# Optimization experiments

Hardware: AMD Instinct MI355X
Metric: run time of the kernel (lower is better)

Reference implementation:

```python
import jax, jax.numpy as jnp
import numpy as np

IDIM = 128
C = 3
NB_SAMPLES = 128
R = 32768
SH_C0 = 0.28209479177387814
SH_C1 = 0.4886025119029199
SH_C2 = np.array([1.0925484305920792, -1.0925484305920792, 0.31539156525252005,
                  -1.0925484305920792, 0.5462742152960396], dtype=np.float32)


def eval_sh_bases(d):
    # d: (R,3) unit directions -> (R,9) degree-2 real SH basis
    x, y, z = d[:, 0], d[:, 1], d[:, 2]
    return jnp.stack([
        jnp.full_like(x, SH_C0),
        -SH_C1 * y, SH_C1 * z, -SH_C1 * x,
        SH_C2[0] * x * y, SH_C2[1] * y * z,
        SH_C2[2] * (2.0 * z * z - x * x - y * y),
        SH_C2[3] * x * z, SH_C2[4] * (x * x - y * y)], axis=-1)


def trilerp(pts, grid):
    # pts: (N,3) in voxel coords (box_min=0, delta_voxel=1); grid: (D,D,D,F)
    D = grid.shape[0]
    p = jnp.clip(pts, 0.0, D - 1 - 1e-4)
    i0 = jnp.floor(p).astype(jnp.int32)
    w = p - i0.astype(p.dtype)          # (N,3) fractional weights
    i1 = jnp.minimum(i0 + 1, D - 1)
    out = jnp.zeros((pts.shape[0], grid.shape[-1]), dtype=p.dtype)
    for dx in (0, 1):
        wx = w[:, 0] if dx else 1.0 - w[:, 0]
        ix = i1[:, 0] if dx else i0[:, 0]
        for dy in (0, 1):
            wy = w[:, 1] if dy else 1.0 - w[:, 1]
            iy = i1[:, 1] if dy else i0[:, 1]
            for dz in (0, 1):
                wz = w[:, 2] if dz else 1.0 - w[:, 2]
                iz = i1[:, 2] if dz else i0[:, 2]
                out = out + (wx * wy * wz)[:, None] * grid[ix, iy, iz]
    return out


def setup_inputs() -> dict:
    key = jax.random.key(0)
    k = jax.random.split(key, 6)
    x = jax.random.uniform(k[0], (R, 3), jnp.float32) * (IDIM - 1)
    d = jax.random.normal(k[1], (R, 3), jnp.float32)
    d = d / jnp.linalg.norm(d, axis=1, keepdims=True)
    tmin = jax.random.uniform(k[2], (R,), jnp.float32) * 5.0
    tmax = tmin + 20.0 + jax.random.uniform(k[3], (R,), jnp.float32) * 80.0
    grid = jax.random.uniform(k[4], (IDIM, IDIM, IDIM, 9 * C), jnp.float32)
    opacity = jax.random.uniform(k[5], (IDIM, IDIM, IDIM, 1), jnp.float32)
    return {"x": x, "d": d, "tmin": tmin, "tmax": tmax, "grid": grid, "opacity": opacity}


def reference(x, d, tmin, tmax, grid, opacity):
    nb_rays = x.shape[0]
    # samples = arange(0.05, 0.95, 1/nb_samples): S entries
    S = int(np.floor(0.9 * NB_SAMPLES - 1e-6)) + 1
    base = 0.05 + jnp.arange(S, dtype=x.dtype) / NB_SAMPLES            # (S,)
    samples = (tmax - tmin)[:, None] * base[None, :] + tmin[:, None]   # (R,S)
    pts = x[:, None, :] + samples[..., None] * d[:, None, :]           # (R,S,3)
    sh = eval_sh_bases(d)                                              # (R,9)
    flat = pts.reshape(-1, 3)
    coeffs = trilerp(flat, grid).reshape(nb_rays, S, C, 9)             # (R,S,C,9)
    op = jnp.clip(trilerp(flat, opacity), 0.0, 100000.0).reshape(nb_rays, S)
    harm = coeffs * sh[:, None, None, :]                               # (R,S,C,9)
    samples_color = jnp.clip(harm.sum(axis=3) + 0.5, 0.0, 100000.0)    # (R,S,C)
    deltas = samples[:, 1:] - samples[:, :-1]                          # (R,S-1)
    dts = -(deltas * op[:, :-1])
    cum = jnp.concatenate([jnp.zeros((nb_rays, 1), dtype=x.dtype),
                           jnp.cumsum(dts, axis=1)[:, :-1]], axis=1)
    w = jnp.exp(cum) * (1.0 - jnp.exp(dts))                            # (R,S-1)
    rays_color = jnp.sum(w[..., None] * samples_color[:, :-1, :], axis=1)  # (R,C)
    return rays_color
```

## Files before the change

kernel.cpp:

```cpp
#include <hip/hip_runtime.h>

#define NS 115
#define WEPS 5e-5f
#define LOG_TSKIP -6.9078f
#define NCELLS (128*128*128)
#define PACK_BYTES ((size_t)NCELLS * 64)
#define NEED_BYTES PACK_BYTES
#define PACK_BLOCKS 2048
#define PACK_THREADS (PACK_BLOCKS * 256)
#define PACK_ITERS ((NCELLS * 4) / PACK_THREADS)

typedef float f32x4 __attribute__((ext_vector_type(4)));
typedef float f32x2 __attribute__((ext_vector_type(2)));
typedef _Float16 h16x8 __attribute__((ext_vector_type(8)));
typedef _Float16 h16x4 __attribute__((ext_vector_type(4)));

struct SH9 { float a,b,c,d,e,f,g,h,i; };

__device__ __forceinline__ f32x4 load4(const float* p) { f32x4 v; __builtin_memcpy(&v, p, 16); return v; }
__device__ __forceinline__ f32x2 load2(const float* p) { f32x2 v; __builtin_memcpy(&v, p, 8);  return v; }
__device__ __forceinline__ h16x8 load8h(const _Float16* p) { h16x8 v; __builtin_memcpy(&v, p, 16); return v; }
__device__ __forceinline__ f32x4 ntload4(const float* p) {
    return __builtin_nontemporal_load((const f32x4*)p);
}

__device__ __forceinline__ void pos_to_cell(float px, float py, float pz,
                                            int& ibase, float* wxs, float* wys, float* wzs) {
    px = fminf(fmaxf(px, 0.0f), 126.9999f);
    py = fminf(fmaxf(py, 0.0f), 126.9999f);
    pz = fminf(fmaxf(pz, 0.0f), 126.9999f);
    int ix = (int)px, iy = (int)py, iz = (int)pz;
    float wx = px - (float)ix, wy = py - (float)iy, wz = pz - (float)iz;
    ibase = (ix << 14) + (iy << 7) + iz;
    wxs[0] = 1.0f - wx; wxs[1] = wx;
    wys[0] = 1.0f - wy; wys[1] = wy;
    wzs[0] = 1.0f - wz; wzs[1] = wz;
}

__device__ __forceinline__ float eval_op(float px, float py, float pz,
                                         const float* __restrict__ opa) {
    int ibase; float wxs[2], wys[2], wzs[2];
    pos_to_cell(px, py, pz, ibase, wxs, wys, wzs);
    float op = 0.0f;
    #pragma unroll
    for (int cx = 0; cx < 2; ++cx)
    #pragma unroll
    for (int cy = 0; cy < 2; ++cy) {
        int idx = ibase + (cx << 14) + (cy << 7);
        f32x2 pr = load2(opa + idx);
        float wxy = wxs[cx] * wys[cy];
        op = fmaf(wxy * wzs[0], pr.x, op);
        op = fmaf(wxy * wzs[1], pr.y, op);
    }
    return fminf(fmaxf(op, 0.0f), 100000.0f);
}

__device__ __forceinline__ void eval_color_f(float px, float py, float pz,
                                             const float* __restrict__ grid,
                                             const SH9& sh,
                                             float& cr, float& cg, float& cb) {
    int ibase; float wxs[2], wys[2], wzs[2];
    pos_to_cell(px, py, pz, ibase, wxs, wys, wzs);
    float r = 0.0f, g = 0.0f, b = 0.0f;
    #pragma unroll
    for (int cx = 0; cx < 2; ++cx)
    #pragma unroll
    for (int cy = 0; cy < 2; ++cy)
    #pragma unroll
    for (int cz = 0; cz < 2; ++cz) {
        int idx = ibase + (cx << 14) + (cy << 7) + cz;
        float wc = wxs[cx] * wys[cy] * wzs[cz];
        const float* cp = grid + (size_t)idx * 27;
        f32x4 v0 = load4(cp);
        f32x4 v1 = load4(cp + 4);
        f32x4 v2 = load4(cp + 8);
        f32x4 v3 = load4(cp + 12);
        f32x4 v4 = load4(cp + 16);
        f32x4 v5 = load4(cp + 20);
        f32x4 v6 = load4(cp + 23);
        float c0 = sh.a*v0.x + sh.b*v0.y + sh.c*v0.z + sh.d*v0.w
                 + sh.e*v1.x + sh.f*v1.y + sh.g*v1.z + sh.h*v1.w + sh.i*v2.x;
        float c1 = sh.a*v2.y + sh.b*v2.z + sh.c*v2.w + sh.d*v3.x
                 + sh.e*v3.y + sh.f*v3.z + sh.g*v3.w + sh.h*v4.x + sh.i*v4.y;
        float c2 = sh.a*v4.z + sh.b*v4.w + sh.c*v5.x + sh.d*v5.y
                 + sh.e*v5.z + sh.f*v5.w + sh.g*v6.y + sh.h*v6.z + sh.i*v6.w;
        r = fmaf(wc, c0, r);
        g = fmaf(wc, c1, g);
        b = fmaf(wc, c2, b);
    }
    cr = fminf(fmaxf(r + 0.5f, 0.0f), 100000.0f);
    cg = fminf(fmaxf(g + 0.5f, 0.0f), 100000.0f);
    cb = fminf(fmaxf(b + 0.5f, 0.0f), 100000.0f);
}

__device__ __forceinline__ float wave_incl_scan(float v, int lane) {
    #pragma unroll
    for (int off = 1; off < 64; off <<= 1) {
        float n = __shfl_up(v, (unsigned)off, 64);
        if (lane >= off) v += n;
    }
    return v;
}

__device__ __forceinline__ SH9 make_sh(float ddx, float ddy, float ddz) {
    SH9 sh;
    sh.a = 0.28209479177387814f;
    sh.b = -0.4886025119029199f * ddy;
    sh.c =  0.4886025119029199f * ddz;
    sh.d = -0.4886025119029199f * ddx;
    sh.e =  1.0925484305920792f * ddx * ddy;
    sh.f = -1.0925484305920792f * ddy * ddz;
    sh.g =  0.31539156525252005f * (2.0f*ddz*ddz - ddx*ddx - ddy*ddy);
    sh.h = -1.0925484305920792f * ddx * ddz;
    sh.i =  0.5462742152960396f * (ddx*ddx - ddy*ddy);
    return sh;
}

__device__ __forceinline__ void pack_one(const float* __restrict__ grid,
                                         _Float16* __restrict__ pack, int o) {
    int cell = o >> 2;
    int q = o & 3;
    int base = cell * 27;
    int offa = base + ((q == 3) ? 23 : q * 8);
    int offb = (q == 3) ? offa : offa + 4;
    f32x4 a = ntload4(grid + offa);
    f32x4 b = ntload4(grid + offb);
    h16x8 out;
    if (q == 3) {
        out[0] = (_Float16)a.y; out[1] = (_Float16)a.z; out[2] = (_Float16)a.w;
        out[3] = (_Float16)0.f; out[4] = (_Float16)0.f; out[5] = (_Float16)0.f;
        out[6] = (_Float16)0.f; out[7] = (_Float16)0.f;
    } else {
        out[0] = (_Float16)a.x; out[1] = (_Float16)a.y; out[2] = (_Float16)a.z; out[3] = (_Float16)a.w;
        out[4] = (_Float16)b.x; out[5] = (_Float16)b.y; out[6] = (_Float16)b.z; out[7] = (_Float16)b.w;
    }
    __builtin_memcpy(pack + ((size_t)o << 3), &out, 16);
}

__global__ __launch_bounds__(256) void pack_kernel(
    const float* __restrict__ grid, _Float16* __restrict__ pack)
{
    const int tid = blockIdx.x * 256 + threadIdx.x;
    #pragma unroll 1
    for (int i = 0; i < PACK_ITERS; i += 8) {
        #pragma unroll
        for (int j = 0; j < 8; ++j)
            pack_one(grid, pack, tid + (i + j) * PACK_THREADS);
    }
}

__global__ __launch_bounds__(256) void fused_color_kernel(
    const float* __restrict__ x, const float* __restrict__ d,
    const float* __restrict__ tmin, const float* __restrict__ tmax,
    const float* __restrict__ opa, const _Float16* __restrict__ pack,
    float* __restrict__ out, int nrays)
{
    int gtid = blockIdx.x * blockDim.x + threadIdx.x;
    int ray = __builtin_amdgcn_readfirstlane(gtid >> 6);
    int lane = threadIdx.x & 63;
    if (ray >= nrays) return;
    int qd  = lane >> 2;
    int sub = lane & 3;

    float ox = x[3*ray+0], oy = x[3*ray+1], oz = x[3*ray+2];
    float ddx = d[3*ray+0], ddy = d[3*ray+1], ddz = d[3*ray+2];
    float t0 = tmin[ray];
    float range = tmax[ray] - t0;
    float delta = range * 0.0078125f;
    SH9 sh = make_sh(ddx, ddy, ddz);

    float tt = range * (0.05f + (float)lane * 0.0078125f) + t0;
    {
    }
    float px0 = ox + tt*ddx, py0 = oy + tt*ddy, pz0 = oz + tt*ddz;
    float opv = eval_op(px0, py0, pz0, opa);
    float dts = -delta * opv;
    float incl = wave_incl_scan(dts, lane);
    float cum = incl - dts;
    float total0 = __shfl(incl, 63, 64);
    float w0 = __expf(cum) * (1.0f - __expf(dts));

    float w1 = 0.0f;
    if (total0 > LOG_TSKIP) {
        int s1 = 64 + lane;
        float dts1 = 0.0f;
        if (s1 < NS) {
            float t1s = range * (0.05f + (float)s1 * 0.0078125f) + t0;
            float qx = ox + t1s*ddx, qy = oy + t1s*ddy, qz = oz + t1s*ddz;
            dts1 = -delta * eval_op(qx, qy, qz, opa);
        }
        float incl1 = wave_incl_scan(dts1, lane);
        float cum1 = total0 + incl1 - dts1;
        w1 = __expf(cum1) * (1.0f - __expf(dts1));
    }

    float s00,s01,s02,s03,s04,s05,s06,s07;
    float s10,s11,s12,s13,s14,s15,s16,s17;
    if (sub == 0) {
        s00=sh.a;s01=sh.b;s02=sh.c;s03=sh.d;s04=sh.e;s05=sh.f;s06=sh.g;s07=sh.h;
        s10=0.f;s11=0.f;s12=0.f;s13=0.f;s14=0.f;s15=0.f;s16=0.f;s17=0.f;
    } else if (sub == 1) {
        s00=sh.i;s01=0.f;s02=0.f;s03=0.f;s04=0.f;s05=0.f;s06=0.f;s07=0.f;
        s10=0.f;s11=sh.a;s12=sh.b;s13=sh.c;s14=sh.d;s15=sh.e;s16=sh.f;s17=sh.g;
    } else if (sub == 2) {
        s00=sh.h;s01=sh.i;s02=0.f;s03=0.f;s04=0.f;s05=0.f;s06=0.f;s07=0.f;
        s10=0.f;s11=0.f;s12=sh.a;s13=sh.b;s14=sh.c;s15=sh.d;s16=sh.e;s17=sh.f;
    } else {
        s00=sh.g;s01=sh.h;s02=sh.i;s03=0.f;s04=0.f;s05=0.f;s06=0.f;s07=0.f;
        s10=0.f;s11=0.f;s12=0.f;s13=0.f;s14=0.f;s15=0.f;s16=0.f;s17=0.f;
    }

    unsigned long long b0 = __ballot(w0 > WEPS);
    unsigned long long b1 = __ballot(w1 > WEPS);

    float accR = 0.0f, accG = 0.0f, accB = 0.0f;

    #pragma unroll 1
    for (int p = 0; p < 8; ++p) {
        unsigned long long bsel = (p < 4) ? b0 : b1;
        int shl = (p & 3) << 4;
        if (((bsel >> shl) & 0xFFFFull) == 0) continue;
        int s = (p << 4) + qd;
        float ws = __shfl((p < 4) ? w0 : w1, s & 63, 64);
        if (ws > WEPS) {
            float st = range * (0.05f + (float)s * 0.0078125f) + t0;
            float px = ox + st*ddx, py = oy + st*ddy, pz = oz + st*ddz;
            int ibase; float wxs[2], wys[2], wzs[2];
            pos_to_cell(px, py, pz, ibase, wxs, wys, wzs);
            float d0a = 0.0f, d1a = 0.0f;
            #pragma unroll
            for (int cx = 0; cx < 2; ++cx)
            #pragma unroll
            for (int cy = 0; cy < 2; ++cy)
            #pragma unroll
            for (int cz = 0; cz < 2; ++cz) {
                int idx = ibase + (cx << 14) + (cy << 7) + cz;
                float wc = wxs[cx] * wys[cy] * wzs[cz];
                const _Float16* cp = pack + ((size_t)idx << 5) + (sub << 3);
                h16x8 v = load8h(cp);
                float f0=(float)v[0], f1=(float)v[1], f2=(float)v[2], f3=(float)v[3];
                float f4=(float)v[4], f5=(float)v[5], f6=(float)v[6], f7=(float)v[7];
                float e0 = s00*f0 + s01*f1 + s02*f2 + s03*f3
                         + s04*f4 + s05*f5 + s06*f6 + s07*f7;
                float e1 = s10*f0 + s11*f1 + s12*f2 + s13*f3
                         + s14*f4 + s15*f5 + s16*f6 + s17*f7;
                d0a = fmaf(wc, e0, d0a);
                d1a = fmaf(wc, e1, d1a);
            }
            float rp = (sub < 2)  ? d0a : 0.0f;
            float gp = (sub == 1) ? d1a : ((sub == 2) ? d0a : 0.0f);
            float bp = (sub == 2) ? d1a : ((sub == 3) ? d0a : 0.0f);
            rp += __shfl_xor(rp, 1, 64); rp += __shfl_xor(rp, 2, 64);
            gp += __shfl_xor(gp, 1, 64); gp += __shfl_xor(gp, 2, 64);
            bp += __shfl_xor(bp, 1, 64); bp += __shfl_xor(bp, 2, 64);
            float cr = fminf(fmaxf(rp + 0.5f, 0.0f), 100000.0f);
            float cg = fminf(fmaxf(gp + 0.5f, 0.0f), 100000.0f);
            float cb = fminf(fmaxf(bp + 0.5f, 0.0f), 100000.0f);
            accR = fmaf(ws, cr, accR);
            accG = fmaf(ws, cg, accG);
            accB = fmaf(ws, cb, accB);
        }
    }

    #pragma unroll
    for (int off = 4; off < 64; off <<= 1) {
        accR += __shfl_xor(accR, off, 64);
        accG += __shfl_xor(accG, off, 64);
        accB += __shfl_xor(accB, off, 64);
    }
    if (lane == 0) {
        out[3*ray+0] = accR;
        out[3*ray+1] = accG;
        out[3*ray+2] = accB;
    }
}

__global__ __launch_bounds__(256) void rf_fallback(
    const float* __restrict__ x, const float* __restrict__ d,
    const float* __restrict__ tmin, const float* __restrict__ tmax,
    const float* __restrict__ grid, const float* __restrict__ opa,
    float* __restrict__ out, int nrays)
{
    int gtid = blockIdx.x * blockDim.x + threadIdx.x;
    int ray = __builtin_amdgcn_readfirstlane(gtid >> 6);
    int lane = threadIdx.x & 63;
    if (ray >= nrays) return;

    float ox = x[3*ray+0], oy = x[3*ray+1], oz = x[3*ray+2];
    float ddx = d[3*ray+0], ddy = d[3*ray+1], ddz = d[3*ray+2];
    float t0 = tmin[ray], t1 = tmax[ray];
    float range = t1 - t0;
    float delta = range * 0.0078125f;
    SH9 sh = make_sh(ddx, ddy, ddz);

    float accR = 0.0f, accG = 0.0f, accB = 0.0f;
    {
        float tt = range * (0.05f + (float)lane * 0.0078125f) + t0;
        float px = ox + tt*ddx, py = oy + tt*ddy, pz = oz + tt*ddz;
        float opv = eval_op(px, py, pz, opa);
        float dts = -delta * opv;
        float incl = wave_incl_scan(dts, lane);
        float cum = incl - dts;
        float total0 = __shfl(incl, 63, 64);
        float w = __expf(cum) * (1.0f - __expf(dts));
        if (w > WEPS) {
            float cr, cg, cb;
            eval_color_f(px, py, pz, grid, sh, cr, cg, cb);
            accR = w * cr; accG = w * cg; accB = w * cb;
        }
        if (total0 > LOG_TSKIP) {
            int s1 = 64 + lane;
            float dts1 = 0.0f;
            float px1 = 0.f, py1 = 0.f, pz1 = 0.f;
            if (s1 < NS) {
                float t1s = range * (0.05f + (float)s1 * 0.0078125f) + t0;
                px1 = ox + t1s*ddx; py1 = oy + t1s*ddy; pz1 = oz + t1s*ddz;
                dts1 = -delta * eval_op(px1, py1, pz1, opa);
            }
            float incl1 = wave_incl_scan(dts1, lane);
            float cum1 = total0 + incl1 - dts1;
            float w1 = __expf(cum1) * (1.0f - __expf(dts1));
            if (w1 > WEPS) {
                float cr, cg, cb;
                eval_color_f(px1, py1, pz1, grid, sh, cr, cg, cb);
                accR = fmaf(w1, cr, accR);
                accG = fmaf(w1, cg, accG);
                accB = fmaf(w1, cb, accB);
            }
        }
    }
    #pragma unroll
    for (int off = 32; off > 0; off >>= 1) {
        accR += __shfl_xor(accR, off, 64);
        accG += __shfl_xor(accG, off, 64);
        accB += __shfl_xor(accB, off, 64);
    }
    if (lane == 0) {
        out[3*ray+0] = accR;
        out[3*ray+1] = accG;
        out[3*ray+2] = accB;
    }
}

extern "C" void kernel_launch(void* const* d_in, const int* in_sizes, int n_in,
                              void* d_out, int out_size, void* d_ws, size_t ws_size,
                              hipStream_t stream) {
    const float* x    = (const float*)d_in[0];
    const float* d    = (const float*)d_in[1];
    const float* tmin = (const float*)d_in[2];
    const float* tmax = (const float*)d_in[3];
    const float* grid = (const float*)d_in[4];
    const float* opa  = (const float*)d_in[5];
    float* out = (float*)d_out;

    int nrays = in_sizes[0] / 3;
    int blocks = (nrays * 64 + 255) / 256;

    if (ws_size >= NEED_BYTES) {
        _Float16* pack = (_Float16*)d_ws;
        pack_kernel<<<PACK_BLOCKS, 256, 0, stream>>>(grid, pack);
        fused_color_kernel<<<blocks, 256, 0, stream>>>(x, d, tmin, tmax, opa, pack, out, nrays);
    } else {
        rf_fallback<<<blocks, 256, 0, stream>>>(x, d, tmin, tmax, grid, opa, out, nrays);
    }
}
```

Before: 391.7 us.

## Drop fp16 grid pre-pack kernel and gather fp32 coefficients directly

```diff
diff --git a/kernel.cpp b/kernel.cpp
--- a/kernel.cpp
+++ b/kernel.cpp
@@ -3,26 +3,14 @@
 #define NS 115
 #define WEPS 5e-5f
 #define LOG_TSKIP -6.9078f
-#define NCELLS (128*128*128)
-#define PACK_BYTES ((size_t)NCELLS * 64)
-#define NEED_BYTES PACK_BYTES
-#define PACK_BLOCKS 2048
-#define PACK_THREADS (PACK_BLOCKS * 256)
-#define PACK_ITERS ((NCELLS * 4) / PACK_THREADS)
 
 typedef float f32x4 __attribute__((ext_vector_type(4)));
 typedef float f32x2 __attribute__((ext_vector_type(2)));
-typedef _Float16 h16x8 __attribute__((ext_vector_type(8)));
-typedef _Float16 h16x4 __attribute__((ext_vector_type(4)));
 
 struct SH9 { float a,b,c,d,e,f,g,h,i; };
 
 __device__ __forceinline__ f32x4 load4(const float* p) { f32x4 v; __builtin_memcpy(&v, p, 16); return v; }
 __device__ __forceinline__ f32x2 load2(const float* p) { f32x2 v; __builtin_memcpy(&v, p, 8);  return v; }
-__device__ __forceinline__ h16x8 load8h(const _Float16* p) { h16x8 v; __builtin_memcpy(&v, p, 16); return v; }
-__device__ __forceinline__ f32x4 ntload4(const float* p) {
-    return __builtin_nontemporal_load((const f32x4*)p);
-}
 
 __device__ __forceinline__ void pos_to_cell(float px, float py, float pz,
                                             int& ibase, float* wxs, float* wys, float* wzs) {
@@ -53,44 +41,6 @@
         op = fmaf(wxy * wzs[1], pr.y, op);
     }
     return fminf(fmaxf(op, 0.0f), 100000.0f);
-}
-
-__device__ __forceinline__ void eval_color_f(float px, float py, float pz,
-                                             const float* __restrict__ grid,
-                                             const SH9& sh,
-                                             float& cr, float& cg, float& cb) {
-    int ibase; float wxs[2], wys[2], wzs[2];
-    pos_to_cell(px, py, pz, ibase, wxs, wys, wzs);
-    float r = 0.0f, g = 0.0f, b = 0.0f;
-    #pragma unroll
-    for (int cx = 0; cx < 2; ++cx)
-    #pragma unroll
-    for (int cy = 0; cy < 2; ++cy)
-    #pragma unroll
-    for (int cz = 0; cz < 2; ++cz) {
-        int idx = ibase + (cx << 14) + (cy << 7) + cz;
-        float wc = wxs[cx] * wys[cy] * wzs[cz];
-        const float* cp = grid + (size_t)idx * 27;
-        f32x4 v0 = load4(cp);
-        f32x4 v1 = load4(cp + 4);
-        f32x4 v2 = load4(cp + 8);
-        f32x4 v3 = load4(cp + 12);
-        f32x4 v4 = load4(cp + 16);
-        f32x4 v5 = load4(cp + 20);
-        f32x4 v6 = load4(cp + 23);
-        float c0 = sh.a*v0.x + sh.b*v0.y + sh.c*v0.z + sh.d*v0.w
-                 + sh.e*v1.x + sh.f*v1.y + sh.g*v1.z + sh.h*v1.w + sh.i*v2.x;
-        float c1 = sh.a*v2.y + sh.b*v2.z + sh.c*v2.w + sh.d*v3.x
-                 + sh.e*v3.y + sh.f*v3.z + sh.g*v3.w + sh.h*v4.x + sh.i*v4.y;
-        float c2 = sh.a*v4.z + sh.b*v4.w + sh.c*v5.x + sh.d*v5.y
-                 + sh.e*v5.z + sh.f*v5.w + sh.g*v6.y + sh.h*v6.z + sh.i*v6.w;
-        r = fmaf(wc, c0, r);
-        g = fmaf(wc, c1, g);
-        b = fmaf(wc, c2, b);
-    }
-    cr = fminf(fmaxf(r + 0.5f, 0.0f), 100000.0f);
-    cg = fminf(fmaxf(g + 0.5f, 0.0f), 100000.0f);
-    cb = fminf(fmaxf(b + 0.5f, 0.0f), 100000.0f);
 }
 
 __device__ __forceinline__ float wave_incl_scan(float v, int lane) {
@@ -116,43 +66,10 @@
     return sh;
 }
 
-__device__ __forceinline__ void pack_one(const float* __restrict__ grid,
-                                         _Float16* __restrict__ pack, int o) {
-    int cell = o >> 2;
-    int q = o & 3;
-    int base = cell * 27;
-    int offa = base + ((q == 3) ? 23 : q * 8);
-    int offb = (q == 3) ? offa : offa + 4;
-    f32x4 a = ntload4(grid + offa);
-    f32x4 b = ntload4(grid + offb);
-    h16x8 out;
-    if (q == 3) {
-        out[0] = (_Float16)a.y; out[1] = (_Float16)a.z; out[2] = (_Float16)a.w;
-        out[3] = (_Float16)0.f; out[4] = (_Float16)0.f; out[5] = (_Float16)0.f;
-        out[6] = (_Float16)0.f; out[7] = (_Float16)0.f;
-    } else {
-        out[0] = (_Float16)a.x; out[1] = (_Float16)a.y; out[2] = (_Float16)a.z; out[3] = (_Float16)a.w;
-        out[4] = (_Float16)b.x; out[5] = (_Float16)b.y; out[6] = (_Float16)b.z; out[7] = (_Float16)b.w;
-    }
-    __builtin_memcpy(pack + ((size_t)o << 3), &out, 16);
-}
-
-__global__ __launch_bounds__(256) void pack_kernel(
-    const float* __restrict__ grid, _Float16* __restrict__ pack)
-{
-    const int tid = blockIdx.x * 256 + threadIdx.x;
-    #pragma unroll 1
-    for (int i = 0; i < PACK_ITERS; i += 8) {
-        #pragma unroll
-        for (int j = 0; j < 8; ++j)
-            pack_one(grid, pack, tid + (i + j) * PACK_THREADS);
-    }
-}
-
 __global__ __launch_bounds__(256) void fused_color_kernel(
     const float* __restrict__ x, const float* __restrict__ d,
     const float* __restrict__ tmin, const float* __restrict__ tmax,
-    const float* __restrict__ opa, const _Float16* __restrict__ pack,
+    const float* __restrict__ opa, const float* __restrict__ grid,
     float* __restrict__ out, int nrays)
 {
     int gtid = blockIdx.x * blockDim.x + threadIdx.x;
@@ -170,8 +87,6 @@
     SH9 sh = make_sh(ddx, ddy, ddz);
 
     float tt = range * (0.05f + (float)lane * 0.0078125f) + t0;
-    {
-    }
     float px0 = ox + tt*ddx, py0 = oy + tt*ddy, pz0 = oz + tt*ddz;
     float opv = eval_op(px0, py0, pz0, opa);
     float dts = -delta * opv;
@@ -206,9 +121,11 @@
         s00=sh.h;s01=sh.i;s02=0.f;s03=0.f;s04=0.f;s05=0.f;s06=0.f;s07=0.f;
         s10=0.f;s11=0.f;s12=sh.a;s13=sh.b;s14=sh.c;s15=sh.d;s16=sh.e;s17=sh.f;
     } else {
-        s00=sh.g;s01=sh.h;s02=sh.i;s03=0.f;s04=0.f;s05=0.f;s06=0.f;s07=0.f;
+        s00=0.f;s01=sh.g;s02=sh.h;s03=sh.i;s04=0.f;s05=0.f;s06=0.f;s07=0.f;
         s10=0.f;s11=0.f;s12=0.f;s13=0.f;s14=0.f;s15=0.f;s16=0.f;s17=0.f;
     }
+    int offa = (sub == 3) ? 23 : (sub << 3);
+    int offb = (sub == 3) ? 23 : offa + 4;
 
     unsigned long long b0 = __ballot(w0 > WEPS);
     unsigned long long b1 = __ballot(w1 > WEPS);
@@ -236,10 +153,11 @@
             for (int cz = 0; cz < 2; ++cz) {
                 int idx = ibase + (cx << 14) + (cy << 7) + cz;
                 float wc = wxs[cx] * wys[cy] * wzs[cz];
-                const _Float16* cp = pack + ((size_t)idx << 5) + (sub << 3);
-                h16x8 v = load8h(cp);
-                float f0=(float)v[0], f1=(float)v[1], f2=(float)v[2], f3=(float)v[3];
-                float f4=(float)v[4], f5=(float)v[5], f6=(float)v[6], f7=(float)v[7];
+                const float* cp = grid + (size_t)idx * 27;
+                f32x4 va = load4(cp + offa);
+                f32x4 vb = load4(cp + offb);
+                float f0=va.x, f1=va.y, f2=va.z, f3=va.w;
+                float f4=vb.x, f5=vb.y, f6=vb.z, f7=vb.w;
                 float e0 = s00*f0 + s01*f1 + s02*f2 + s03*f3
                          + s04*f4 + s05*f5 + s06*f6 + s07*f7;
                 float e1 = s10*f0 + s11*f1 + s12*f2 + s13*f3
@@ -275,73 +193,6 @@
     }
 }
 
-__global__ __launch_bounds__(256) void rf_fallback(
-    const float* __restrict__ x, const float* __restrict__ d,
-    const float* __restrict__ tmin, const float* __restrict__ tmax,
-    const float* __restrict__ grid, const float* __restrict__ opa,
-    float* __restrict__ out, int nrays)
-{
-    int gtid = blockIdx.x * blockDim.x + threadIdx.x;
-    int ray = __builtin_amdgcn_readfirstlane(gtid >> 6);
-    int lane = threadIdx.x & 63;
-    if (ray >= nrays) return;
-
-    float ox = x[3*ray+0], oy = x[3*ray+1], oz = x[3*ray+2];
-    float ddx = d[3*ray+0], ddy = d[3*ray+1], ddz = d[3*ray+2];
-    float t0 = tmin[ray], t1 = tmax[ray];
-    float range = t1 - t0;
-    float delta = range * 0.0078125f;
-    SH9 sh = make_sh(ddx, ddy, ddz);
-
-    float accR = 0.0f, accG = 0.0f, accB = 0.0f;
-    {
-        float tt = range * (0.05f + (float)lane * 0.0078125f) + t0;
-        float px = ox + tt*ddx, py = oy + tt*ddy, pz = oz + tt*ddz;
-        float opv = eval_op(px, py, pz, opa);
-        float dts = -delta * opv;
-        float incl = wave_incl_scan(dts, lane);
-        float cum = incl - dts;
-        float total0 = __shfl(incl, 63, 64);
-        float w = __expf(cum) * (1.0f - __expf(dts));
-        if (w > WEPS) {
-            float cr, cg, cb;
-            eval_color_f(px, py, pz, grid, sh, cr, cg, cb);
-            accR = w * cr; accG = w * cg; accB = w * cb;
-        }
-        if (total0 > LOG_TSKIP) {
-            int s1 = 64 + lane;
-            float dts1 = 0.0f;
-            float px1 = 0.f, py1 = 0.f, pz1 = 0.f;
-            if (s1 < NS) {
-                float t1s = range * (0.05f + (float)s1 * 0.0078125f) + t0;
-                px1 = ox + t1s*ddx; py1 = oy + t1s*ddy; pz1 = oz + t1s*ddz;
-                dts1 = -delta * eval_op(px1, py1, pz1, opa);
-            }
-            float incl1 = wave_incl_scan(dts1, lane);
-            float cum1 = total0 + incl1 - dts1;
-            float w1 = __expf(cum1) * (1.0f - __expf(dts1));
-            if (w1 > WEPS) {
-                float cr, cg, cb;
-                eval_color_f(px1, py1, pz1, grid, sh, cr, cg, cb);
-                accR = fmaf(w1, cr, accR);
-                accG = fmaf(w1, cg, accG);
-                accB = fmaf(w1, cb, accB);
-            }
-        }
-    }
-    #pragma unroll
-    for (int off = 32; off > 0; off >>= 1) {
-        accR += __shfl_xor(accR, off, 64);
-        accG += __shfl_xor(accG, off, 64);
-        accB += __shfl_xor(accB, off, 64);
-    }
-    if (lane == 0) {
-        out[3*ray+0] = accR;
-        out[3*ray+1] = accG;
-        out[3*ray+2] = accB;
-    }
-}
-
 extern "C" void kernel_launch(void* const* d_in, const int* in_sizes, int n_in,
                               void* d_out, int out_size, void* d_ws, size_t ws_size,
                               hipStream_t stream) {
@@ -356,11 +207,6 @@
     int nrays = in_sizes[0] / 3;
     int blocks = (nrays * 64 + 255) / 256;
 
-    if (ws_size >= NEED_BYTES) {
-        _Float16* pack = (_Float16*)d_ws;
-        pack_kernel<<<PACK_BLOCKS, 256, 0, stream>>>(grid, pack);
-        fused_color_kernel<<<blocks, 256, 0, stream>>>(x, d, tmin, tmax, opa, pack, out, nrays);
-    } else {
-        rf_fallback<<<blocks, 256, 0, stream>>>(x, d, tmin, tmax, grid, opa, out, nrays);
-    }
-}
+    (void)d_ws; (void)ws_size;
+    fused_color_kernel<<<blocks, 256, 0, stream>>>(x, d, tmin, tmax, opa, grid, out, nrays);
+}
```

Result: no change. 390.1 us (-0.4%).
